# Kernel optimization log

Measured on AMD Instinct MI355X. Metric: run time of the kernel, lower is better.

Reference implementation:

```python
import jax, jax.numpy as jnp
import numpy as np

NUM_INST = 3
N_NODES = 50000
IN_F = 128
HID = 64
HEADS = 4
HF = HEADS * HID  # 256
NEG_SLOPE = 0.2
BN_EPS = 1e-5


def setup_inputs() -> dict:
    key = jax.random.key(0)
    ks = jax.random.split(key, 10)
    sppmi = jax.random.normal(ks[0], (NUM_INST, N_NODES, IN_F), dtype=jnp.float32)
    edge_index = jax.random.randint(ks[1], (2, 800000), 0, N_NODES, dtype=jnp.int64)
    # Per-instance GATConv params (lin_src weight, att_src/att_dst, bias), BN, and Linear
    s = 1.0 / np.sqrt(IN_F)
    W = jax.random.uniform(ks[2], (NUM_INST, HF, IN_F), jnp.float32, -s, s)
    att_src = jax.random.uniform(ks[3], (NUM_INST, HEADS, HID), jnp.float32, -s, s)
    att_dst = jax.random.uniform(ks[4], (NUM_INST, HEADS, HID), jnp.float32, -s, s)
    bias = jnp.zeros((NUM_INST, HF), jnp.float32)
    bn_gamma = jnp.ones((NUM_INST, HF), jnp.float32)
    bn_beta = jnp.zeros((NUM_INST, HF), jnp.float32)
    bn_mean = jnp.zeros((NUM_INST, HF), jnp.float32)
    bn_var = jnp.ones((NUM_INST, HF), jnp.float32)
    s2 = 1.0 / np.sqrt(HF)
    lin_W = jax.random.uniform(ks[5], (NUM_INST, HID, HF), jnp.float32, -s2, s2)
    lin_b = jax.random.uniform(ks[6], (NUM_INST, HID), jnp.float32, -s2, s2)
    return {"sppmi": sppmi, "W": W, "att_src": att_src, "att_dst": att_dst,
            "bias": bias, "bn_gamma": bn_gamma, "bn_beta": bn_beta,
            "bn_mean": bn_mean, "bn_var": bn_var, "lin_W": lin_W,
            "lin_b": lin_b, "edge_index": edge_index}


def _gat_layer(x, W, a_src, a_dst, bias, gamma, beta, mean, var, linW, linb, src, dst):
    # GATConv (concat=True, add_self_loops already applied via src/dst)
    xw = (x @ W.T).reshape(N_NODES, HEADS, HID)            # [N,H,F]
    alpha_src = (xw * a_src).sum(-1)                        # [N,H]
    alpha_dst = (xw * a_dst).sum(-1)                        # [N,H]
    e = jax.nn.leaky_relu(alpha_src[src] + alpha_dst[dst], NEG_SLOPE)  # [E,H]
    m = jax.ops.segment_max(e, dst, num_segments=N_NODES)  # segment softmax over dst
    e = jnp.exp(e - m[dst])
    denom = jax.ops.segment_sum(e, dst, num_segments=N_NODES)
    alpha = e / (denom[dst] + 1e-16)                        # [E,H]
    msg = alpha[:, :, None] * xw[src]                       # [E,H,F] gather-attend
    out = jax.ops.segment_sum(msg, dst, num_segments=N_NODES)  # scatter-add
    out = out.reshape(N_NODES, HF) + bias
    # BatchNorm1d (eval: running stats), ReLU, Linear
    out = (out - mean) * jax.lax.rsqrt(var + BN_EPS) * gamma + beta
    out = jax.nn.relu(out)
    return out @ linW.T + linb                              # [N,HID]


def reference(sppmi, W, att_src, att_dst, bias, bn_gamma, bn_beta, bn_mean, bn_var, lin_W, lin_b, edge_index):
    loop = jnp.arange(N_NODES, dtype=edge_index.dtype)
    src = jnp.concatenate([edge_index[0], loop])
    dst = jnp.concatenate([edge_index[1], loop])
    all_emb = jnp.zeros((N_NODES, HID), jnp.float32)
    for i in range(NUM_INST):
        all_emb = all_emb + _gat_layer(sppmi[i], W[i], att_src[i], att_dst[i], bias[i],
                                       bn_gamma[i], bn_beta[i], bn_mean[i], bn_var[i],
                                       lin_W[i], lin_b[i], src, dst)
    out_1 = all_emb / jnp.linalg.norm(all_emb, axis=1, keepdims=True)
    return out_1
```

## Files before the change

### kernel.cpp

```cpp
#include <hip/hip_runtime.h>
#include <hip/hip_bf16.h>

#define N_NODES 50000
#define E0      800000
#define ET      850000
#define IN_F    128
#define HF      256
#define HID     64
#define NEG     0.2f
#define BN_EPSC 1e-5f
#define NSCAN_BLK 196

typedef __attribute__((ext_vector_type(8))) short bh8;
typedef __attribute__((ext_vector_type(4))) float fl4;
typedef __attribute__((ext_vector_type(8))) unsigned short us8;

__device__ __forceinline__ float lrelu(float x){ return x > 0.f ? x : NEG * x; }
__device__ __forceinline__ unsigned short f2b(float f){
  unsigned int x = __float_as_uint(f);
  unsigned int r = x + 0x7FFF + ((x >> 16) & 1);
  return (unsigned short)(r >> 16);
}
__device__ __forceinline__ float b2f(unsigned short u){
  return __uint_as_float((unsigned int)u << 16);
}

#define NW4 (3 * HF * IN_F / 4)
#define NL4 (3 * HID * HF / 4)
__global__ __launch_bounds__(256) void k_prep(const float* __restrict__ W, unsigned short* __restrict__ wb,
                                              const float* __restrict__ linW, unsigned short* __restrict__ lwb,
                                              const float* __restrict__ g, const float* __restrict__ b,
                                              const float* __restrict__ m, const float* __restrict__ v,
                                              float* __restrict__ scale, float* __restrict__ shiftv){
  int idx = blockIdx.x * 256 + threadIdx.x;
  if (idx < NW4){
    float4 x = ((const float4*)W)[idx];
    ((ushort4*)wb)[idx] = make_ushort4(f2b(x.x), f2b(x.y), f2b(x.z), f2b(x.w));
  } else if (idx < NW4 + NL4){
    int j = idx - NW4;
    float4 x = ((const float4*)linW)[j];
    ((ushort4*)lwb)[j] = make_ushort4(f2b(x.x), f2b(x.y), f2b(x.z), f2b(x.w));
  } else if (idx < NW4 + NL4 + 3 * HF){
    int i = idx - NW4 - NL4;
    float s = g[i] * rsqrtf(v[i] + BN_EPSC);
    scale[i] = s;
    shiftv[i] = b[i] - m[i] * s;
  }
}

__global__ void k_hist(const int* __restrict__ ei, int* __restrict__ counts){
  int e = blockIdx.x * 256 + threadIdx.x;
  if (e >= ET) return;
  int d = (e < E0) ? ei[E0 + e] : (e - E0);
  atomicAdd(&counts[d], 1);
}

__global__ __launch_bounds__(256) void k_bsum(const int* __restrict__ counts, int* __restrict__ bsums){
  int b = blockIdx.x;
  int t = threadIdx.x;
  int idx = b * 256 + t;
  int v = (idx < N_NODES) ? counts[idx] : 0;
  for (int m = 1; m < 64; m <<= 1) v += __shfl_xor(v, m, 64);
  __shared__ int ws[4];
  int lane = t & 63, w = t >> 6;
  if (lane == 0) ws[w] = v;
  __syncthreads();
  if (t == 0) bsums[b] = ws[0] + ws[1] + ws[2] + ws[3];
}

__global__ __launch_bounds__(256) void k_bscan(const int* __restrict__ bsums, int* __restrict__ bexcl,
                                               int* __restrict__ row_ptr){
  int t = threadIdx.x;
  int v = (t < NSCAN_BLK) ? bsums[t] : 0;
  int lane = t & 63, w = t >> 6;
  int incl = v;
  for (int m = 1; m < 64; m <<= 1){
    int n = __shfl_up(incl, m, 64);
    if (lane >= m) incl += n;
  }
  __shared__ int ws[4];
  if (lane == 63) ws[w] = incl;
  __syncthreads();
  if (t == 0){
    int r = 0;
    for (int j = 0; j < 4; ++j){ int x = ws[j]; ws[j] = r; r += x; }
  }
  __syncthreads();
  int excl = incl - v + ws[w];
  if (t < NSCAN_BLK) bexcl[t] = excl;
  if (t == 255) row_ptr[N_NODES] = excl + v;
}

__global__ __launch_bounds__(256) void k_sfinal(const int* __restrict__ counts,
                                                const int* __restrict__ bexcl,
                                                int* __restrict__ row_ptr, int* __restrict__ cursor){
  int b = blockIdx.x;
  int t = threadIdx.x;
  int idx = b * 256 + t;
  int v = (idx < N_NODES) ? counts[idx] : 0;
  int lane = t & 63, w = t >> 6;
  int incl = v;
  for (int m = 1; m < 64; m <<= 1){
    int n = __shfl_up(incl, m, 64);
    if (lane >= m) incl += n;
  }
  __shared__ int ws[4];
  if (lane == 63) ws[w] = incl;
  __syncthreads();
  if (t == 0){
    int r = 0;
    for (int j = 0; j < 4; ++j){ int x = ws[j]; ws[j] = r; r += x; }
  }
  __syncthreads();
  int excl = incl - v + ws[w];
  int pos = bexcl[b] + excl;
  if (idx < N_NODES){ row_ptr[idx] = pos; cursor[idx] = pos; }
}

__global__ void k_scatter(const int* __restrict__ ei, int* __restrict__ cursor,
                          int* __restrict__ csr_src){
  int e = blockIdx.x * 256 + threadIdx.x;
  if (e >= ET) return;
  int s, d;
  if (e < E0){ s = ei[e]; d = ei[E0 + e]; } else { s = e - E0; d = s; }
  int pos = atomicAdd(&cursor[d], 1);
  csr_src[pos] = s;
}

__global__ __launch_bounds__(256) void k_gemm1f(const float* __restrict__ sppmi,
                                                const unsigned short* __restrict__ wb,
                                                const float* __restrict__ att_src,
                                                const float* __restrict__ att_dst,
                                                unsigned short* __restrict__ xwb,
                                                float* __restrict__ as3, float* __restrict__ ad3){
  __shared__ unsigned char Asm[64 * 256];
  int tid = threadIdx.x;
  int bx = blockIdx.x;
  int inst = bx / 782;
  int m0 = (bx % 782) * 64;
  const float* x = sppmi + (size_t)inst * N_NODES * IN_F;
  const unsigned short* wbv = wb + (size_t)inst * HF * IN_F;
  const float* asrc = att_src + inst * HF;
  const float* adst = att_dst + inst * HF;
  float* as_ = as3 + (size_t)inst * N_NODES * 4;
  float* ad_ = ad3 + (size_t)inst * N_NODES * 4;
  unsigned short* xw = xwb + (size_t)inst * N_NODES * HF;

  #pragma unroll
  for (int k = 0; k < 8; ++k){
    int c = k * 256 + tid;
    int row = c >> 5;
    int c4 = c & 31;
    int grow = m0 + row; if (grow >= N_NODES) grow = N_NODES - 1;
    float4 v = *(const float4*)&x[(size_t)grow * IN_F + c4 * 4];
    ushort4 o = make_ushort4(f2b(v.x), f2b(v.y), f2b(v.z), f2b(v.w));
    int colb = c4 * 8;
    int addr = row * 256 + ((colb & ~15) ^ ((row & 7) << 4)) + (colb & 15);
    *(ushort4*)(Asm + addr) = o;
  }
  __syncthreads();

  int w = tid >> 6, lane = tid & 63;
  int l15 = lane & 15, l4 = lane >> 4;
  const char* bbase = (const char*)wbv + (size_t)(w * 64 + l15) * 256 + l4 * 16;
  fl4 acc[4][4] = {};
  #pragma unroll
  for (int kk = 0; kk < 4; ++kk){
    bh8 bfv[4];
    #pragma unroll
    for (int n = 0; n < 4; ++n)
      bfv[n] = *(const bh8*)(bbase + n * 16 * 256 + kk * 64);
    bh8 af[4];
    #pragma unroll
    for (int m = 0; m < 4; ++m){
      int ar = m * 16 + l15;
      int ac = (kk * 64 + l4 * 16) ^ ((ar & 7) << 4);
      af[m] = *(const bh8*)(Asm + ar * 256 + ac);
    }
    #pragma unroll
    for (int m = 0; m < 4; ++m)
      #pragma unroll
      for (int n = 0; n < 4; ++n)
        acc[m][n] = __builtin_amdgcn_mfma_f32_16x16x32_bf16(af[m], bfv[n], acc[m][n], 0, 0, 0);
  }

  float asv[4], adv[4];
  #pragma unroll
  for (int n = 0; n < 4; ++n){
    int c = w * 64 + n * 16 + l15;
    asv[n] = asrc[c]; adv[n] = adst[c];
  }

  #pragma unroll
  for (int m = 0; m < 4; ++m){
    #pragma unroll
    for (int j = 0; j < 4; ++j){
      int grow = m0 + m * 16 + l4 * 4 + j;
      if (grow < N_NODES){
        #pragma unroll
        for (int n = 0; n < 4; ++n)
          xw[(size_t)grow * HF + w * 64 + n * 16 + l15] = f2b(acc[m][n][j]);
      }
      float ts = acc[m][0][j]*asv[0] + acc[m][1][j]*asv[1] + acc[m][2][j]*asv[2] + acc[m][3][j]*asv[3];
      float td = acc[m][0][j]*adv[0] + acc[m][1][j]*adv[1] + acc[m][2][j]*adv[2] + acc[m][3][j]*adv[3];
      #pragma unroll
      for (int mm = 1; mm < 16; mm <<= 1){ ts += __shfl_xor(ts, mm, 64); td += __shfl_xor(td, mm, 64); }
      if (l15 == 0 && grow < N_NODES){
        as_[grow * 4 + w] = ts;
        ad_[grow * 4 + w] = td;
      }
    }
  }
}

__global__ __launch_bounds__(256) void k_agg3(const unsigned short* __restrict__ xwb,
                     const float* __restrict__ as3, const float* __restrict__ ad3,
                     const int* __restrict__ row_ptr, const int* __restrict__ csr_src,
                     const float* __restrict__ bias, unsigned short* __restrict__ outb){
  __shared__ float eLds[4][4][65];
  __shared__ int   sLds[4][64];
  int bx = blockIdx.x;
  int inst = bx / 12500;
  int chunk = bx - inst * 12500;
  int w = threadIdx.x >> 6;
  int lane = threadIdx.x & 63;
  int node = chunk * 4 + w;
  int row0 = row_ptr[node];
  int deg = row_ptr[node + 1] - row0;
  const float* as_ = as3 + (size_t)inst * N_NODES * 4;
  const float* ad_ = ad3 + (size_t)inst * N_NODES * 4;
  float4 ad4 = *(const float4*)&ad_[node * 4];
  int h = lane >> 4;
  float accx = 0.f, accy = 0.f, accz = 0.f, accw = 0.f;
  float sh;
  const char* xwp = (const char*)(xwb + (size_t)inst * N_NODES * HF);
  int lb = lane * 8;

  if (deg <= 64){
    int soff = 0; float e0 = 0.f, e1 = 0.f, e2 = 0.f, e3 = 0.f;
    if (lane < deg){
      int sreg = csr_src[row0 + lane];
      soff = sreg * 512;
      float4 a4 = *(const float4*)&as_[sreg * 4];
      e0 = __expf(lrelu(a4.x + ad4.x));
      e1 = __expf(lrelu(a4.y + ad4.y));
      e2 = __expf(lrelu(a4.z + ad4.z));
      e3 = __expf(lrelu(a4.w + ad4.w));
    }
    sLds[w][lane] = soff;
    eLds[w][0][lane] = e0; eLds[w][1][lane] = e1;
    eLds[w][2][lane] = e2; eLds[w][3][lane] = e3;
    float s0 = e0, s1 = e1, s2 = e2, s3 = e3;
    for (int m = 1; m < 64; m <<= 1){
      s0 += __shfl_xor(s0, m, 64); s1 += __shfl_xor(s1, m, 64);
      s2 += __shfl_xor(s2, m, 64); s3 += __shfl_xor(s3, m, 64);
    }
    sh = (h == 0) ? s0 : (h == 1) ? s1 : (h == 2) ? s2 : s3;
    int q = 0;
    for (; q + 4 <= deg; q += 4){
      int o0 = sLds[w][q],   o1 = sLds[w][q+1];
      int o2 = sLds[w][q+2], o3 = sLds[w][q+3];
      float w0 = eLds[w][h][q],   w1 = eLds[w][h][q+1];
      float w2 = eLds[w][h][q+2], w3 = eLds[w][h][q+3];
      ushort4 u0 = *(const ushort4*)(xwp + o0 + lb);
      ushort4 u1 = *(const ushort4*)(xwp + o1 + lb);
      ushort4 u2 = *(const ushort4*)(xwp + o2 + lb);
      ushort4 u3 = *(const ushort4*)(xwp + o3 + lb);
      accx += w0*b2f(u0.x) + w1*b2f(u1.x) + w2*b2f(u2.x) + w3*b2f(u3.x);
      accy += w0*b2f(u0.y) + w1*b2f(u1.y) + w2*b2f(u2.y) + w3*b2f(u3.y);
      accz += w0*b2f(u0.z) + w1*b2f(u1.z) + w2*b2f(u2.z) + w3*b2f(u3.z);
      accw += w0*b2f(u0.w) + w1*b2f(u1.w) + w2*b2f(u2.w) + w3*b2f(u3.w);
    }
    for (; q < deg; ++q){
      int o0 = sLds[w][q];
      float wh = eLds[w][h][q];
      ushort4 u = *(const ushort4*)(xwp + o0 + lb);
      accx += wh * b2f(u.x); accy += wh * b2f(u.y);
      accz += wh * b2f(u.z); accw += wh * b2f(u.w);
    }
  } else {
    float s0 = 0.f, s1 = 0.f, s2 = 0.f, s3 = 0.f;
    for (int j = lane; j < deg; j += 64){
      int s = csr_src[row0 + j];
      float4 a4 = *(const float4*)&as_[s * 4];
      s0 += __expf(lrelu(a4.x + ad4.x));
      s1 += __expf(lrelu(a4.y + ad4.y));
      s2 += __expf(lrelu(a4.z + ad4.z));
      s3 += __expf(lrelu(a4.w + ad4.w));
    }
    for (int m = 1; m < 64; m <<= 1){
      s0 += __shfl_xor(s0, m, 64); s1 += __shfl_xor(s1, m, 64);
      s2 += __shfl_xor(s2, m, 64); s3 += __shfl_xor(s3, m, 64);
    }
    sh = (h == 0) ? s0 : (h == 1) ? s1 : (h == 2) ? s2 : s3;
    for (int jb = 0; jb < deg; jb += 64){
      int jj = jb + lane;
      int soff = 0; float e0 = 0.f, e1 = 0.f, e2 = 0.f, e3 = 0.f;
      if (jj < deg){
        int sreg = csr_src[row0 + jj];
        soff = sreg * 512;
        float4 a4 = *(const float4*)&as_[sreg * 4];
        e0 = __expf(lrelu(a4.x + ad4.x));
        e1 = __expf(lrelu(a4.y + ad4.y));
        e2 = __expf(lrelu(a4.z + ad4.z));
        e3 = __expf(lrelu(a4.w + ad4.w));
      }
      sLds[w][lane] = soff;
      eLds[w][0][lane] = e0; eLds[w][1][lane] = e1;
      eLds[w][2][lane] = e2; eLds[w][3][lane] = e3;
      __builtin_amdgcn_s_waitcnt(0);
      int lim = min(64, deg - jb);
      for (int q = 0; q < lim; ++q){
        int o0 = sLds[w][q];
        float wh = eLds[w][h][q];
        ushort4 u = *(const ushort4*)(xwp + o0 + lb);
        accx += wh * b2f(u.x); accy += wh * b2f(u.y);
        accz += wh * b2f(u.z); accw += wh * b2f(u.w);
      }
    }
  }
  float invh = 1.f / (sh + 1e-16f);
  const float* bi = bias + inst * HF;
  float4 b4 = *(const float4*)&bi[lane * 4];
  ushort4 o;
  o.x = f2b(accx * invh + b4.x); o.y = f2b(accy * invh + b4.y);
  o.z = f2b(accz * invh + b4.z); o.w = f2b(accw * invh + b4.w);
  *(ushort4*)&outb[(size_t)inst * N_NODES * HF + (size_t)node * HF + lane * 4] = o;
}

__global__ __launch_bounds__(256) void k_gemm2f(const unsigned short* __restrict__ obase,
                                                const unsigned short* __restrict__ lwb,
                                                const float* __restrict__ scale,
                                                const float* __restrict__ shiftv,
                                                const float* __restrict__ linb,
                                                float* __restrict__ outp){
  __shared__ unsigned char Asm[64 * 512];
  int tid = threadIdx.x;
  int m0 = blockIdx.x * 64;
  int w = tid >> 6, lane = tid & 63;
  int l15 = lane & 15, l4 = lane >> 4;

  fl4 acc[4] = {};

  for (int i = 0; i < 3; ++i){
    if (i) __syncthreads();
    const unsigned short* A = obase + (size_t)i * N_NODES * HF;
    const float* sc = scale + i * HF;
    const float* sf = shiftv + i * HF;
    #pragma unroll
    for (int k = 0; k < 8; ++k){
      int c = k * 256 + tid;
      int row = c >> 5;
      int colb = (c & 31) * 16;
      int col = colb >> 1;
      int grow = m0 + row; if (grow >= N_NODES) grow = N_NODES - 1;
      us8 u = *(const us8*)&A[(size_t)grow * HF + col];
      float4 s0 = *(const float4*)&sc[col], s1 = *(const float4*)&sc[col + 4];
      float4 f0 = *(const float4*)&sf[col], f1 = *(const float4*)&sf[col + 4];
      us8 o;
      o[0] = f2b(fmaxf(0.f, b2f(u[0]) * s0.x + f0.x));
      o[1] = f2b(fmaxf(0.f, b2f(u[1]) * s0.y + f0.y));
      o[2] = f2b(fmaxf(0.f, b2f(u[2]) * s0.z + f0.z));
      o[3] = f2b(fmaxf(0.f, b2f(u[3]) * s0.w + f0.w));
      o[4] = f2b(fmaxf(0.f, b2f(u[4]) * s1.x + f1.x));
      o[5] = f2b(fmaxf(0.f, b2f(u[5]) * s1.y + f1.y));
      o[6] = f2b(fmaxf(0.f, b2f(u[6]) * s1.z + f1.z));
      o[7] = f2b(fmaxf(0.f, b2f(u[7]) * s1.w + f1.w));
      *(us8*)(Asm + row * 512 + (colb ^ ((row & 7) << 4))) = o;
    }
    __syncthreads();
    const char* bbase = (const char*)(lwb + (size_t)i * HID * HF) + (size_t)l15 * 512 + l4 * 16;
    #pragma unroll
    for (int kk = 0; kk < 8; ++kk){
      int ar = w * 16 + l15;
      int ac = (kk * 64 + l4 * 16) ^ ((ar & 7) << 4);
      bh8 af = *(const bh8*)(Asm + ar * 512 + ac);
      #pragma unroll
      for (int n = 0; n < 4; ++n){
        bh8 bfv = *(const bh8*)(bbase + n * 16 * 512 + kk * 64);
        acc[n] = __builtin_amdgcn_mfma_f32_16x16x32_bf16(af, bfv, acc[n], 0, 0, 0);
      }
    }
  }
  float lbs[4];
  #pragma unroll
  for (int n = 0; n < 4; ++n){
    int c = n * 16 + l15;
    lbs[n] = linb[c] + linb[64 + c] + linb[128 + c];
  }
  #pragma unroll
  for (int j = 0; j < 4; ++j){
    float v0 = acc[0][j] + lbs[0];
    float v1 = acc[1][j] + lbs[1];
    float v2 = acc[2][j] + lbs[2];
    float v3 = acc[3][j] + lbs[3];
    float ss = v0*v0 + v1*v1 + v2*v2 + v3*v3;
    #pragma unroll
    for (int mm = 1; mm < 16; mm <<= 1) ss += __shfl_xor(ss, mm, 64);
    float rn = 1.f / sqrtf(ss);
    int grow = m0 + w * 16 + l4 * 4 + j;
    if (grow < N_NODES){
      float* op = outp + (size_t)grow * HID;
      op[l15]      = v0 * rn;
      op[16 + l15] = v1 * rn;
      op[32 + l15] = v2 * rn;
      op[48 + l15] = v3 * rn;
    }
  }
}

extern "C" void kernel_launch(void* const* d_in, const int* in_sizes, int n_in,
                              void* d_out, int out_size, void* d_ws, size_t ws_size,
                              hipStream_t stream){
  const float* sppmi   = (const float*)d_in[0];
  const float* W       = (const float*)d_in[1];
  const float* att_src = (const float*)d_in[2];
  const float* att_dst = (const float*)d_in[3];
  const float* bias    = (const float*)d_in[4];
  const float* bn_g    = (const float*)d_in[5];
  const float* bn_b    = (const float*)d_in[6];
  const float* bn_m    = (const float*)d_in[7];
  const float* bn_v    = (const float*)d_in[8];
  const float* lin_W   = (const float*)d_in[9];
  const float* lin_b   = (const float*)d_in[10];
  const int*   ei      = (const int*)d_in[11];

  char* ws = (char*)d_ws;
  size_t off = 0;
  auto alloc = [&](size_t bytes)->char*{ char* p = ws + off; off += (bytes + 255) & ~(size_t)255; return p; };
  unsigned short* wb   = (unsigned short*)alloc((size_t)3 * HF * IN_F * 2);
  unsigned short* lwb  = (unsigned short*)alloc((size_t)3 * HID * HF * 2);
  float* scale  = (float*)alloc((size_t)3 * HF * 4);
  float* shiftv = (float*)alloc((size_t)3 * HF * 4);
  unsigned short* xwb  = (unsigned short*)alloc((size_t)3 * N_NODES * HF * 2);
  unsigned short* outb = (unsigned short*)alloc((size_t)3 * N_NODES * HF * 2);
  float* as3    = (float*)alloc((size_t)3 * N_NODES * 4 * 4);
  float* ad3    = (float*)alloc((size_t)3 * N_NODES * 4 * 4);
  int* counts   = (int*)alloc((size_t)N_NODES * 4);
  int* row_ptr  = (int*)alloc((size_t)(N_NODES + 4) * 4);
  int* cursor   = (int*)alloc((size_t)N_NODES * 4);
  int* csr      = (int*)alloc((size_t)ET * 4);
  int* bsums    = (int*)alloc((size_t)NSCAN_BLK * 4);
  int* bexcl    = (int*)alloc((size_t)NSCAN_BLK * 4);

  hipMemsetAsync(counts, 0, (size_t)N_NODES * 4, stream);

  k_prep<<<147, 256, 0, stream>>>(W, wb, lin_W, lwb, bn_g, bn_b, bn_m, bn_v, scale, shiftv);

  k_hist<<<(ET + 255) / 256, 256, 0, stream>>>(ei, counts);
  k_bsum<<<NSCAN_BLK, 256, 0, stream>>>(counts, bsums);
  k_bscan<<<1, 256, 0, stream>>>(bsums, bexcl, row_ptr);
  k_sfinal<<<NSCAN_BLK, 256, 0, stream>>>(counts, bexcl, row_ptr, cursor);
  k_scatter<<<(ET + 255) / 256, 256, 0, stream>>>(ei, cursor, csr);

  k_gemm1f<<<3 * 782, 256, 0, stream>>>(sppmi, wb, att_src, att_dst, xwb, as3, ad3);
  k_agg3<<<37500, 256, 0, stream>>>(xwb, as3, ad3, row_ptr, csr, bias, outb);
  k_gemm2f<<<782, 256, 0, stream>>>(outb, lwb, scale, shiftv, lin_b, (float*)d_out);
}
```

Before: 393.7 us.

## Stage weight tiles in LDS and halve GEMM1 row tile

```diff
diff --git a/kernel.cpp b/kernel.cpp
--- a/kernel.cpp
+++ b/kernel.cpp
@@ -133,11 +133,12 @@
                                                 const float* __restrict__ att_dst,
                                                 unsigned short* __restrict__ xwb,
                                                 float* __restrict__ as3, float* __restrict__ ad3){
-  __shared__ unsigned char Asm[64 * 256];
+  __shared__ unsigned char Asm[32 * 256];
+  __shared__ unsigned char Bsm[256 * 256];
   int tid = threadIdx.x;
   int bx = blockIdx.x;
-  int inst = bx / 782;
-  int m0 = (bx % 782) * 64;
+  int inst = bx / 1563;
+  int m0 = (bx % 1563) * 32;
   const float* x = sppmi + (size_t)inst * N_NODES * IN_F;
   const unsigned short* wbv = wb + (size_t)inst * HF * IN_F;
   const float* asrc = att_src + inst * HF;
@@ -147,7 +148,7 @@
   unsigned short* xw = xwb + (size_t)inst * N_NODES * HF;
 
   #pragma unroll
-  for (int k = 0; k < 8; ++k){
+  for (int k = 0; k < 4; ++k){
     int c = k * 256 + tid;
     int row = c >> 5;
     int c4 = c & 31;
@@ -158,27 +159,37 @@
     int addr = row * 256 + ((colb & ~15) ^ ((row & 7) << 4)) + (colb & 15);
     *(ushort4*)(Asm + addr) = o;
   }
+  #pragma unroll
+  for (int k = 0; k < 16; ++k){
+    int c = k * 256 + tid;
+    int row = c >> 4;
+    int colb = (c & 15) * 16;
+    uint4 v = *(const uint4*)((const char*)wbv + (size_t)row * 256 + colb);
+    *(uint4*)(Bsm + row * 256 + (colb ^ ((row & 7) << 4))) = v;
+  }
   __syncthreads();
 
   int w = tid >> 6, lane = tid & 63;
   int l15 = lane & 15, l4 = lane >> 4;
-  const char* bbase = (const char*)wbv + (size_t)(w * 64 + l15) * 256 + l4 * 16;
-  fl4 acc[4][4] = {};
+  fl4 acc[2][4] = {};
   #pragma unroll
   for (int kk = 0; kk < 4; ++kk){
-    bh8 bfv[4];
-    #pragma unroll
-    for (int n = 0; n < 4; ++n)
-      bfv[n] = *(const bh8*)(bbase + n * 16 * 256 + kk * 64);
-    bh8 af[4];
-    #pragma unroll
-    for (int m = 0; m < 4; ++m){
+    bh8 af[2];
+    #pragma unroll
+    for (int m = 0; m < 2; ++m){
       int ar = m * 16 + l15;
       int ac = (kk * 64 + l4 * 16) ^ ((ar & 7) << 4);
       af[m] = *(const bh8*)(Asm + ar * 256 + ac);
     }
-    #pragma unroll
-    for (int m = 0; m < 4; ++m)
+    bh8 bfv[4];
+    #pragma unroll
+    for (int n = 0; n < 4; ++n){
+      int br = w * 64 + n * 16 + l15;
+      int bc = (kk * 64 + l4 * 16) ^ ((br & 7) << 4);
+      bfv[n] = *(const bh8*)(Bsm + br * 256 + bc);
+    }
+    #pragma unroll
+    for (int m = 0; m < 2; ++m)
       #pragma unroll
       for (int n = 0; n < 4; ++n)
         acc[m][n] = __builtin_amdgcn_mfma_f32_16x16x32_bf16(af[m], bfv[n], acc[m][n], 0, 0, 0);
@@ -192,7 +203,7 @@
   }
 
   #pragma unroll
-  for (int m = 0; m < 4; ++m){
+  for (int m = 0; m < 2; ++m){
     #pragma unroll
     for (int j = 0; j < 4; ++j){
       int grow = m0 + m * 16 + l4 * 4 + j;
@@ -335,6 +346,7 @@
                                                 const float* __restrict__ linb,
                                                 float* __restrict__ outp){
   __shared__ unsigned char Asm[64 * 512];
+  __shared__ unsigned char Bsm[64 * 512];
   int tid = threadIdx.x;
   int m0 = blockIdx.x * 64;
   int w = tid >> 6, lane = tid & 63;
@@ -368,8 +380,16 @@
       o[7] = f2b(fmaxf(0.f, b2f(u[7]) * s1.w + f1.w));
       *(us8*)(Asm + row * 512 + (colb ^ ((row & 7) << 4))) = o;
     }
+    const unsigned short* B = lwb + (size_t)i * HID * HF;
+    #pragma unroll
+    for (int k = 0; k < 8; ++k){
+      int c = k * 256 + tid;
+      int row = c >> 5;
+      int colb = (c & 31) * 16;
+      uint4 v = *(const uint4*)((const char*)B + (size_t)row * 512 + colb);
+      *(uint4*)(Bsm + row * 512 + (colb ^ ((row & 7) << 4))) = v;
+    }
     __syncthreads();
-    const char* bbase = (const char*)(lwb + (size_t)i * HID * HF) + (size_t)l15 * 512 + l4 * 16;
     #pragma unroll
     for (int kk = 0; kk < 8; ++kk){
       int ar = w * 16 + l15;
@@ -377,7 +397,9 @@
       bh8 af = *(const bh8*)(Asm + ar * 512 + ac);
       #pragma unroll
       for (int n = 0; n < 4; ++n){
-        bh8 bfv = *(const bh8*)(bbase + n * 16 * 512 + kk * 64);
+        int br = n * 16 + l15;
+        int bc = (kk * 64 + l4 * 16) ^ ((br & 7) << 4);
+        bh8 bfv = *(const bh8*)(Bsm + br * 512 + bc);
         acc[n] = __builtin_amdgcn_mfma_f32_16x16x32_bf16(af, bfv, acc[n], 0, 0, 0);
       }
     }
@@ -453,7 +475,7 @@
   k_sfinal<<<NSCAN_BLK, 256, 0, stream>>>(counts, bexcl, row_ptr, cursor);
   k_scatter<<<(ET + 255) / 256, 256, 0, stream>>>(ei, cursor, csr);
 
-  k_gemm1f<<<3 * 782, 256, 0, stream>>>(sppmi, wb, att_src, att_dst, xwb, as3, ad3);
+  k_gemm1f<<<3 * 1563, 256, 0, stream>>>(sppmi, wb, att_src, att_dst, xwb, as3, ad3);
   k_agg3<<<37500, 256, 0, stream>>>(xwb, as3, ad3, row_ptr, csr, bias, outb);
   k_gemm2f<<<782, 256, 0, stream>>>(outb, lwb, scale, shiftv, lin_b, (float*)d_out);
 }
```

Result: faster. 361.2 us (-8.2%).
